# Optimization experiments

Hardware: AMD Instinct MI355X
Metric: run time of the kernel (lower is better)

The kernel has to match this reference:

```python
import jax, jax.numpy as jnp
import numpy as np
from jax import lax

BN_EPS = 1e-5


def _conv(x, w, b):
    # 3x3 conv, stride 1, padding 1 (SAME), NCHW/OIHW
    y = lax.conv_general_dilated(x, w, (1, 1), 'SAME',
                                 dimension_numbers=('NCHW', 'OIHW', 'NCHW'))
    return y + b[None, :, None, None]


def _bn(x, g, b, m, v):
    # eval-mode batchnorm with running stats
    scale = (g / jnp.sqrt(v + BN_EPS))[None, :, None, None]
    return (x - m[None, :, None, None]) * scale + b[None, :, None, None]


def _pool(x):
    # MaxPool2d(2,2), VALID (floor division of spatial dims)
    return lax.reduce_window(x, -jnp.inf, lax.max, (1, 1, 2, 2), (1, 1, 2, 2), 'VALID')


def _quantum(xq, qp):
    """Batched 5-qubit statevector sim of the PennyLane circuit.
    Wire i: RX(xq[:, i%2]) then RY(qp[i%2]); CNOT(0,1); CNOT(1,2); <Z0 Z1>.
    xq: [B, 32] (only first 2 features used). Returns [B] float32.
    """
    B = xq.shape[0]
    psi = jnp.zeros((B, 32), jnp.complex64).at[:, 0].set(1.0)
    for i in range(5):  # fixed tiny loop over wires
        a = xq[:, i % 2]          # [B] data angle
        th = qp[i % 2]            # scalar weight angle
        ca, sa = jnp.cos(a * 0.5), jnp.sin(a * 0.5)
        RX = jnp.stack([jnp.stack([ca, -1j * sa], -1),
                        jnp.stack([-1j * sa, ca], -1)], -2).astype(jnp.complex64)  # [B,2,2]
        cb, sb = jnp.cos(th * 0.5), jnp.sin(th * 0.5)
        RY = jnp.stack([jnp.stack([cb, -sb]), jnp.stack([sb, cb])]).astype(jnp.complex64)  # [2,2]
        U = jnp.einsum('ij,bjk->bik', RY, RX)  # [B,2,2] per-wire unitary
        psi = psi.reshape(B, 2 ** i, 2, 2 ** (4 - i))
        psi = jnp.einsum('bij,bajc->baic', U, psi).reshape(B, 32)
    psi = psi.reshape(B, 2, 2, 2, 2, 2)
    # CNOT(0,1): flip qubit 1 where qubit 0 == 1
    psi = psi.at[:, 1].set(psi[:, 1, ::-1])
    # CNOT(1,2): flip qubit 2 where qubit 1 == 1
    psi = psi.at[:, :, 1].set(psi[:, :, 1, ::-1])
    z01 = jnp.array([[1.0, -1.0], [-1.0, 1.0]], jnp.float32).reshape(1, 2, 2, 1, 1, 1)
    prob = jnp.real(psi) ** 2 + jnp.imag(psi) ** 2
    return jnp.sum(prob * z01, axis=(1, 2, 3, 4, 5))


def setup_inputs() -> dict:
    key = jax.random.key(0)
    ks = jax.random.split(key, 24)
    B = 8192
    s = 0.05
    d = {}
    d['x'] = jax.random.normal(ks[0], (B, 1, 28, 28), jnp.float32)
    d['conv1_w'] = jax.random.normal(ks[1], (64, 1, 3, 3), jnp.float32) * s
    d['conv1_b'] = jax.random.normal(ks[2], (64,), jnp.float32) * s
    d['conv2_w'] = jax.random.normal(ks[3], (128, 64, 3, 3), jnp.float32) * s
    d['conv2_b'] = jax.random.normal(ks[4], (128,), jnp.float32) * s
    d['conv3_w'] = jax.random.normal(ks[5], (256, 128, 3, 3), jnp.float32) * s
    d['conv3_b'] = jax.random.normal(ks[6], (256,), jnp.float32) * s
    for i, c in [(1, 64), (2, 128), (3, 256)]:
        d[f'bn{i}_g'] = jnp.ones((c,), jnp.float32)
        d[f'bn{i}_b'] = jnp.zeros((c,), jnp.float32)
        d[f'bn{i}_m'] = jax.random.normal(ks[6 + i], (c,), jnp.float32) * 0.1
        d[f'bn{i}_v'] = jax.random.uniform(ks[9 + i], (c,), jnp.float32, 0.5, 1.5)
    d['fc1_w'] = jax.random.normal(ks[13], (32, 256 * 3 * 3), jnp.float32) * s
    d['fc1_b'] = jax.random.normal(ks[14], (32,), jnp.float32) * s
    d['q_params'] = jax.random.uniform(ks[15], (8,), jnp.float32)
    d['fc2_w'] = jax.random.normal(ks[16], (128, 1), jnp.float32) * s
    d['fc2_b'] = jax.random.normal(ks[17], (128,), jnp.float32) * s
    d['fc3_w'] = jax.random.normal(ks[18], (2, 128), jnp.float32) * s
    d['fc3_b'] = jax.random.normal(ks[19], (2,), jnp.float32) * s
    return d


def reference(x, conv1_w, conv1_b, conv2_w, conv2_b, conv3_w, conv3_b,
              bn1_g, bn1_b, bn1_m, bn1_v, bn2_g, bn2_b, bn2_m, bn2_v,
              bn3_g, bn3_b, bn3_m, bn3_v, fc1_w, fc1_b, q_params,
              fc2_w, fc2_b, fc3_w, fc3_b):
    h = _pool(jax.nn.relu(_bn(_conv(x, conv1_w, conv1_b), bn1_g, bn1_b, bn1_m, bn1_v)))
    h = _pool(jax.nn.relu(_bn(_conv(h, conv2_w, conv2_b), bn2_g, bn2_b, bn2_m, bn2_v)))
    h = _pool(jax.nn.relu(_bn(_conv(h, conv3_w, conv3_b), bn3_g, bn3_b, bn3_m, bn3_v)))
    # dropout is identity in eval mode
    h = h.reshape(h.shape[0], -1)              # [B, 2304]
    h = h @ fc1_w.T + fc1_b                     # [B, 32]
    q = _quantum(h, q_params)[:, None]          # [B, 1]
    h = q @ fc2_w.T + fc2_b                     # [B, 128]
    logits = h @ fc3_w.T + fc3_b                # [B, 2]
    return jax.nn.log_softmax(logits, axis=1)
```

## Files before the change

kernel.cpp:

```cpp
#include <hip/hip_runtime.h>
#include <hip/hip_bf16.h>
#include <math.h>

typedef float f32x4 __attribute__((ext_vector_type(4)));
typedef short s16x8 __attribute__((ext_vector_type(8)));

static const long long OFF_W2  = 0LL;
static const long long OFF_W3  = 147456LL;
static const long long OFF_AB1 = 737280LL;
static const long long OFF_AB2 = 737792LL;
static const long long OFF_AB3 = 738816LL;
static const long long OFF_Q   = 740864LL;

__device__ inline unsigned short f2bfu(float f) {
    __hip_bfloat16 h = __float2bfloat16(f);
    unsigned short u;
    __builtin_memcpy(&u, &h, 2);
    return u;
}

__global__ __launch_bounds__(256) void prep_k(
    const float* __restrict__ c2w, const float* __restrict__ c3w,
    const float* __restrict__ c1b, const float* __restrict__ g1, const float* __restrict__ b1,
    const float* __restrict__ m1, const float* __restrict__ v1,
    const float* __restrict__ c2b, const float* __restrict__ g2, const float* __restrict__ b2,
    const float* __restrict__ m2, const float* __restrict__ v2,
    const float* __restrict__ c3b, const float* __restrict__ g3, const float* __restrict__ b3,
    const float* __restrict__ m3, const float* __restrict__ v3,
    const float* __restrict__ fc1b, const float* __restrict__ qp,
    const float* __restrict__ fc2w, const float* __restrict__ fc2b,
    const float* __restrict__ fc3w, const float* __restrict__ fc3b,
    short* __restrict__ wT2, short* __restrict__ wT3,
    float2* __restrict__ ab1, float2* __restrict__ ab2, float2* __restrict__ ab3,
    float* __restrict__ qc)
{
    int tid = blockIdx.x * 256 + threadIdx.x;
    if (tid < 73728) {
        int ic = tid & 63, oc = (tid >> 6) & 127, k = tid >> 13;
        wT2[tid] = (short)f2bfu(c2w[(oc * 64 + ic) * 9 + k]);
    }
    if (tid < 294912) {
        int ic = tid & 127, oc = (tid >> 7) & 255, k = tid >> 15;
        wT3[tid] = (short)f2bfu(c3w[(oc * 128 + ic) * 9 + k]);
    }
    if (tid < 64) {
        float s = g1[tid] / sqrtf(v1[tid] + 1e-5f);
        ab1[tid] = make_float2(s, (c1b[tid] - m1[tid]) * s + b1[tid]);
    } else if (tid < 192) {
        int c = tid - 64;
        float s = g2[c] / sqrtf(v2[c] + 1e-5f);
        ab2[c] = make_float2(s, (c2b[c] - m2[c]) * s + b2[c]);
    } else if (tid < 448) {
        int c = tid - 192;
        float s = g3[c] / sqrtf(v3[c] + 1e-5f);
        ab3[c] = make_float2(s, (c3b[c] - m3[c]) * s + b3[c]);
    } else if (tid == 448) {
        float A0 = 0.f, A1 = 0.f, B0 = 0.f, B1 = 0.f;
        for (int k = 0; k < 128; ++k) {
            float f2 = fc2w[k], fb = fc2b[k];
            A0 += fc3w[k] * f2;        B0 += fc3w[k] * fb;
            A1 += fc3w[128 + k] * f2;  B1 += fc3w[128 + k] * fb;
        }
        qc[0] = A0; qc[1] = A1;
        qc[2] = B0 + fc3b[0]; qc[3] = B1 + fc3b[1];
        qc[4] = cosf(qp[1]);  qc[5] = fc1b[1];
    }
}

__global__ __launch_bounds__(512, 6) void fused_k(
    const float* __restrict__ x, const float* __restrict__ c1w,
    const float2* __restrict__ ab1, const float2* __restrict__ ab2,
    const float2* __restrict__ ab3,
    const short* __restrict__ wT2, const short* __restrict__ wT3,
    const float* __restrict__ fc1w, const float* __restrict__ qc,
    float* __restrict__ out)
{
    __shared__ short xs2[16 * 16 * 64];
    __shared__ short u3[8 * 8 * 128];

    float (*xt)[32] = (float (*)[32])u3;
    short* xs3 = u3;
    float* red = (float*)u3;

    int b = blockIdx.x, t = threadIdx.x;

    for (int i = t; i < 8192; i += 512) ((unsigned*)xs2)[i] = 0u;
    for (int i = t; i < 960;  i += 512) ((unsigned*)u3)[i] = 0u;
    __syncthreads();

    for (int i = t; i < 784; i += 512) xt[i / 28 + 1][i % 28 + 1] = x[b * 784 + i];

    int ocg = t & 15;
    float wr[4][9];
    float2 abr[4];
#pragma unroll
    for (int c = 0; c < 4; ++c) {
#pragma unroll
        for (int k = 0; k < 9; ++k) wr[c][k] = c1w[(ocg * 4 + c) * 9 + k];
        abr[c] = ab1[ocg * 4 + c];
    }
    __syncthreads();

    int posb = t >> 4;
    for (int p = posb; p < 196; p += 32) {
        int py = p / 14, px = p % 14;
        int y0 = 2 * py, x0 = 2 * px;
        float patch[4][4];
#pragma unroll
        for (int i = 0; i < 4; ++i)
#pragma unroll
            for (int j = 0; j < 4; ++j) patch[i][j] = xt[y0 + i][x0 + j];

        unsigned short ub[4];
#pragma unroll
        for (int c = 0; c < 4; ++c) {
            float a00 = 0.f, a01 = 0.f, a10 = 0.f, a11 = 0.f;
#pragma unroll
            for (int ky = 0; ky < 3; ++ky)
#pragma unroll
                for (int kx = 0; kx < 3; ++kx) {
                    float wv = wr[c][ky * 3 + kx];
                    a00 += patch[ky + 0][kx + 0] * wv;
                    a01 += patch[ky + 0][kx + 1] * wv;
                    a10 += patch[ky + 1][kx + 0] * wv;
                    a11 += patch[ky + 1][kx + 1] * wv;
                }
            float aa = abr[c].x, bb = abr[c].y;
            float v = fmaxf(fmaxf(a00 * aa + bb, a01 * aa + bb),
                            fmaxf(a10 * aa + bb, a11 * aa + bb));
            ub[c] = f2bfu(fmaxf(v, 0.f));
        }
        uint2 pk;
        pk.x = (unsigned)ub[0] | ((unsigned)ub[1] << 16);
        pk.y = (unsigned)ub[2] | ((unsigned)ub[3] << 16);
        int blk = (ocg >> 1) ^ ((px + 1) & 7);
        *(uint2*)&xs2[((((py + 1) * 16) + (px + 1)) * 8 + blk) * 8 + (ocg & 1) * 4] = pk;
    }
    __syncthreads();
    for (int i = t; i < 960; i += 512) {
        int pos = i >> 6, w = i & 63;
        int yy = (pos < 8) ? 0 : pos - 7;
        int xx = (pos < 8) ? pos : 0;
        ((unsigned*)xs3)[(yy * 8 + xx) * 64 + w] = 0u;
    }

    int lane = t & 63, wid = t >> 6;
    int quad = lane >> 4, n16 = lane & 15;
    int dy = n16 >> 3, lx = n16 & 7;

    {
        f32x4 acc[14];
        f32x4 z = {0.f, 0.f, 0.f, 0.f};
#pragma unroll
        for (int nt = 0; nt < 14; ++nt) acc[nt] = z;

#pragma unroll 1
        for (int kykx = 0; kykx < 9; ++kykx) {
            int ky = kykx / 3, kx = kykx - 3 * ky;
            int dyky = dy + ky;
            int xc0 = lx + kx;
            int xc1 = xc0 + 8; if (xc1 > 15) xc1 = 15;
#pragma unroll
            for (int kk = 0; kk < 2; ++kk) {
                s16x8 A = *(const s16x8*)(wT2 + ((kykx * 128 + wid * 16 + n16) * 64 + kk * 32 + quad * 8));
                int bi = kk * 4 + quad;
#pragma unroll
                for (int nt = 0; nt < 14; ++nt) {
                    int ry = nt >> 1, cb = nt & 1;
                    int y_in = 2 * ry + dyky;
                    int x_in = cb ? xc1 : xc0;
                    int blk = bi ^ (x_in & 7);
                    s16x8 B = *(const s16x8*)&xs2[((y_in * 16 + x_in) * 8 + blk) * 8];
                    acc[nt] = __builtin_amdgcn_mfma_f32_16x16x32_bf16(A, B, acc[nt], 0, 0, 0);
                }
            }
        }

        int m = lx >> 1;
        bool keep = (dy == 0) && ((lx & 1) == 0);
        int oc0 = wid * 16 + quad * 4;
        float2 abv[4];
#pragma unroll
        for (int r = 0; r < 4; ++r) abv[r] = ab2[oc0 + r];
#pragma unroll
        for (int nt = 0; nt < 14; ++nt) {
            int ry = nt >> 1, cb = nt & 1;
            int xp = cb * 4 + m;
            float pv[4];
#pragma unroll
            for (int r = 0; r < 4; ++r) {
                float v = acc[nt][r] * abv[r].x + abv[r].y;
                v = fmaxf(v, __shfl_xor(v, 1));
                v = fmaxf(v, __shfl_xor(v, 8));
                pv[r] = fmaxf(v, 0.f);
            }
            if (keep && xp < 7) {
                uint2 pk;
                pk.x = (unsigned)f2bfu(pv[0]) | ((unsigned)f2bfu(pv[1]) << 16);
                pk.y = (unsigned)f2bfu(pv[2]) | ((unsigned)f2bfu(pv[3]) << 16);
                int blk3 = (oc0 >> 3) ^ (((xp + 1) & 7) << 1);
                *(uint2*)&xs3[(((ry + 1) * 8 + (xp + 1)) * 16 + blk3) * 8 + (oc0 & 7)] = pk;
            }
        }
    }
    __syncthreads();

    f32x4 acc[2][3];
    f32x4 z = {0.f, 0.f, 0.f, 0.f};
#pragma unroll
    for (int ml = 0; ml < 2; ++ml)
#pragma unroll
        for (int nt = 0; nt < 3; ++nt) acc[ml][nt] = z;

#pragma unroll 1
    for (int kykx = 0; kykx < 9; ++kykx) {
        int ky = kykx / 3, kx = kykx - 3 * ky;
        int dyky = dy + ky;
        int x_in = lx + kx; if (x_in > 7) x_in = 7;
#pragma unroll
        for (int kk = 0; kk < 4; ++kk) {
            s16x8 A[2];
#pragma unroll
            for (int ml = 0; ml < 2; ++ml)
                A[ml] = *(const s16x8*)(wT3 + ((kykx * 256 + (wid * 2 + ml) * 16 + n16) * 128 + kk * 32 + quad * 8));
            int bi = kk * 4 + quad;
            int blk = bi ^ ((x_in & 7) << 1);
#pragma unroll
            for (int nt = 0; nt < 3; ++nt) {
                int y_in = 2 * nt + dyky;
                s16x8 B = *(const s16x8*)&xs3[((y_in * 8 + x_in) * 16 + blk) * 8];
#pragma unroll
                for (int ml = 0; ml < 2; ++ml)
                    acc[ml][nt] = __builtin_amdgcn_mfma_f32_16x16x32_bf16(A[ml], B, acc[ml][nt], 0, 0, 0);
            }
        }
    }
    __syncthreads();

    float vacc = 0.f;
    int m = lx >> 1;
    bool keep = (dy == 0) && ((lx & 1) == 0) && (m < 3);
    const float* fc1w1 = fc1w + 2304;
#pragma unroll
    for (int ml = 0; ml < 2; ++ml) {
        int oc0 = (wid * 2 + ml) * 16 + quad * 4;
        float2 abv[4];
#pragma unroll
        for (int r = 0; r < 4; ++r) abv[r] = ab3[oc0 + r];
#pragma unroll
        for (int nt = 0; nt < 3; ++nt) {
#pragma unroll
            for (int r = 0; r < 4; ++r) {
                float v = acc[ml][nt][r] * abv[r].x + abv[r].y;
                v = fmaxf(v, __shfl_xor(v, 1));
                v = fmaxf(v, __shfl_xor(v, 8));
                v = fmaxf(v, 0.f);
                if (keep) vacc += v * fc1w1[(oc0 + r) * 9 + nt * 3 + m];
            }
        }
    }
#pragma unroll
    for (int s = 1; s < 64; s <<= 1) vacc += __shfl_xor(vacc, s);
    if (lane == 0) red[wid] = vacc;
    __syncthreads();
    if (t == 0) {
        float v = red[0] + red[1] + red[2] + red[3]
                + red[4] + red[5] + red[6] + red[7] + qc[5];
        float q = cosf(v) * qc[4];
        float l0 = q * qc[0] + qc[2];
        float l1 = q * qc[1] + qc[3];
        float mx = fmaxf(l0, l1);
        float lse = mx + logf(__expf(l0 - mx) + __expf(l1 - mx));
        out[b * 2 + 0] = l0 - lse;
        out[b * 2 + 1] = l1 - lse;
    }
}

extern "C" void kernel_launch(void* const* d_in, const int* in_sizes, int n_in,
                              void* d_out, int out_size, void* d_ws, size_t ws_size,
                              hipStream_t stream)
{
    const float* x    = (const float*)d_in[0];
    const float* c1w  = (const float*)d_in[1];
    const float* c1b  = (const float*)d_in[2];
    const float* c2w  = (const float*)d_in[3];
    const float* c2b  = (const float*)d_in[4];
    const float* c3w  = (const float*)d_in[5];
    const float* c3b  = (const float*)d_in[6];
    const float* g1   = (const float*)d_in[7];
    const float* b1   = (const float*)d_in[8];
    const float* m1   = (const float*)d_in[9];
    const float* v1   = (const float*)d_in[10];
    const float* g2   = (const float*)d_in[11];
    const float* b2   = (const float*)d_in[12];
    const float* m2   = (const float*)d_in[13];
    const float* v2   = (const float*)d_in[14];
    const float* g3   = (const float*)d_in[15];
    const float* b3   = (const float*)d_in[16];
    const float* m3   = (const float*)d_in[17];
    const float* v3   = (const float*)d_in[18];
    const float* fc1w = (const float*)d_in[19];
    const float* fc1b = (const float*)d_in[20];
    const float* qp   = (const float*)d_in[21];
    const float* fc2w = (const float*)d_in[22];
    const float* fc2b = (const float*)d_in[23];
    const float* fc3w = (const float*)d_in[24];
    const float* fc3b = (const float*)d_in[25];
    float* out = (float*)d_out;
    char* ws = (char*)d_ws;

    short*  wT2 = (short*)(ws + OFF_W2);
    short*  wT3 = (short*)(ws + OFF_W3);
    float2* ab1 = (float2*)(ws + OFF_AB1);
    float2* ab2 = (float2*)(ws + OFF_AB2);
    float2* ab3 = (float2*)(ws + OFF_AB3);
    float*  qc  = (float*)(ws + OFF_Q);

    int B = in_sizes[0] / 784;

    prep_k<<<1152, 256, 0, stream>>>(c2w, c3w, c1b, g1, b1, m1, v1,
                                     c2b, g2, b2, m2, v2, c3b, g3, b3, m3, v3,
                                     fc1b, qp, fc2w, fc2b, fc3w, fc3b,
                                     wT2, wT3, ab1, ab2, ab3, qc);
    fused_k<<<B, 512, 0, stream>>>(x, c1w, ab1, ab2, ab3, wT2, wT3, fc1w, qc, out);
}
```

Baseline: 935.2 us.

## Compute conv1 with bf16 MFMA and fold BN into weights

Replaces the scalar FP32 conv1+BN+ReLU+pool loop with a bf16 MFMA 16x16x32 formulation. The BN scale is folded into the weights and the shift enters as a bias row against a constant-one input. The 2x2 max-pool is done with lane shuffles across the MFMA output columns. The input loads are also hoisted before the shared-memory zeroing to overlap latency. This adds bf16 rounding of the input pixels and of the BN-scaled weights, which were previously FP32, so it risks a small accuracy loss.

Measured after the change: 1.289 ms. 1.38x slower.

```diff
diff --git a/kernel.cpp b/kernel.cpp
--- a/kernel.cpp
+++ b/kernel.cpp
@@ -83,58 +83,82 @@
     float* red = (float*)u3;
 
     int b = blockIdx.x, t = threadIdx.x;
+    int lane = t & 63, wid = t >> 6;
+    int n16 = lane & 15, quad = lane >> 4;
+    int dy = n16 >> 3, lx = n16 & 7;
+
+    float xv0 = x[b * 784 + t];
+    float xv1 = (t + 512 < 784) ? x[b * 784 + t + 512] : 0.f;
+
+    s16x8 A1f[4];
+#pragma unroll
+    for (int ot = 0; ot < 4; ++ot) {
+        float2 ab = ab1[ot * 16 + n16];
+        s16x8 a = {0, 0, 0, 0, 0, 0, 0, 0};
+        if (quad == 0) {
+#pragma unroll
+            for (int j = 0; j < 8; ++j)
+                a[j] = (short)f2bfu(c1w[(ot * 16 + n16) * 9 + j] * ab.x);
+        } else if (quad == 1) {
+            a[0] = (short)f2bfu(c1w[(ot * 16 + n16) * 9 + 8] * ab.x);
+            a[1] = (short)f2bfu(ab.y);
+        }
+        A1f[ot] = a;
+    }
 
     for (int i = t; i < 8192; i += 512) ((unsigned*)xs2)[i] = 0u;
     for (int i = t; i < 960;  i += 512) ((unsigned*)u3)[i] = 0u;
     __syncthreads();
 
-    for (int i = t; i < 784; i += 512) xt[i / 28 + 1][i % 28 + 1] = x[b * 784 + i];
-
-    int ocg = t & 15;
-    float wr[4][9];
-    float2 abr[4];
-#pragma unroll
-    for (int c = 0; c < 4; ++c) {
-#pragma unroll
-        for (int k = 0; k < 9; ++k) wr[c][k] = c1w[(ocg * 4 + c) * 9 + k];
-        abr[c] = ab1[ocg * 4 + c];
-    }
-    __syncthreads();
-
-    int posb = t >> 4;
-    for (int p = posb; p < 196; p += 32) {
-        int py = p / 14, px = p % 14;
-        int y0 = 2 * py, x0 = 2 * px;
-        float patch[4][4];
-#pragma unroll
-        for (int i = 0; i < 4; ++i)
-#pragma unroll
-            for (int j = 0; j < 4; ++j) patch[i][j] = xt[y0 + i][x0 + j];
-
-        unsigned short ub[4];
-#pragma unroll
-        for (int c = 0; c < 4; ++c) {
-            float a00 = 0.f, a01 = 0.f, a10 = 0.f, a11 = 0.f;
-#pragma unroll
-            for (int ky = 0; ky < 3; ++ky)
-#pragma unroll
-                for (int kx = 0; kx < 3; ++kx) {
-                    float wv = wr[c][ky * 3 + kx];
-                    a00 += patch[ky + 0][kx + 0] * wv;
-                    a01 += patch[ky + 0][kx + 1] * wv;
-                    a10 += patch[ky + 1][kx + 0] * wv;
-                    a11 += patch[ky + 1][kx + 1] * wv;
-                }
-            float aa = abr[c].x, bb = abr[c].y;
-            float v = fmaxf(fmaxf(a00 * aa + bb, a01 * aa + bb),
-                            fmaxf(a10 * aa + bb, a11 * aa + bb));
-            ub[c] = f2bfu(fmaxf(v, 0.f));
-        }
-        uint2 pk;
-        pk.x = (unsigned)ub[0] | ((unsigned)ub[1] << 16);
-        pk.y = (unsigned)ub[2] | ((unsigned)ub[3] << 16);
-        int blk = (ocg >> 1) ^ ((px + 1) & 7);
-        *(uint2*)&xs2[((((py + 1) * 16) + (px + 1)) * 8 + blk) * 8 + (ocg & 1) * 4] = pk;
+    xt[t / 28 + 1][t % 28 + 1] = xv0;
+    if (t + 512 < 784) xt[(t + 512) / 28 + 1][(t + 512) % 28 + 1] = xv1;
+    __syncthreads();
+
+    for (int T = wid; T < 49; T += 8) {
+        int q = T * 4 + (n16 >> 2);
+        int qy = q / 14, qx = q - qy * 14;
+        int yy = 2 * qy + ((n16 >> 1) & 1);
+        int xx = 2 * qx + (n16 & 1);
+        const float* pxt = &xt[yy][xx];
+        s16x8 Bf = {0, 0, 0, 0, 0, 0, 0, 0};
+        if (quad == 0) {
+            Bf[0] = (short)f2bfu(pxt[0]);
+            Bf[1] = (short)f2bfu(pxt[1]);
+            Bf[2] = (short)f2bfu(pxt[2]);
+            Bf[3] = (short)f2bfu(pxt[32]);
+            Bf[4] = (short)f2bfu(pxt[33]);
+            Bf[5] = (short)f2bfu(pxt[34]);
+            Bf[6] = (short)f2bfu(pxt[64]);
+            Bf[7] = (short)f2bfu(pxt[65]);
+        } else if (quad == 1) {
+            Bf[0] = (short)f2bfu(pxt[66]);
+            Bf[1] = (short)0x3F80;
+        }
+
+        f32x4 z4 = {0.f, 0.f, 0.f, 0.f};
+        bool wr = ((n16 & 3) == 0);
+        int wb = (qy + 1) * 16 + (qx + 1);
+        int blkb = (qx + 1) & 7;
+#pragma unroll
+        for (int ot = 0; ot < 4; ++ot) {
+            f32x4 acc = __builtin_amdgcn_mfma_f32_16x16x32_bf16(A1f[ot], Bf, z4, 0, 0, 0);
+            unsigned short us[4];
+#pragma unroll
+            for (int r = 0; r < 4; ++r) {
+                float v = acc[r];
+                v = fmaxf(v, __shfl_xor(v, 1));
+                v = fmaxf(v, __shfl_xor(v, 2));
+                us[r] = f2bfu(fmaxf(v, 0.f));
+            }
+            if (wr) {
+                int oc0 = ot * 16 + quad * 4;
+                uint2 pk;
+                pk.x = (unsigned)us[0] | ((unsigned)us[1] << 16);
+                pk.y = (unsigned)us[2] | ((unsigned)us[3] << 16);
+                int blk = (oc0 >> 3) ^ blkb;
+                *(uint2*)&xs2[((wb * 8) + blk) * 8 + (oc0 & 7)] = pk;
+            }
+        }
     }
     __syncthreads();
     for (int i = t; i < 960; i += 512) {
@@ -143,10 +167,6 @@
         int xx = (pos < 8) ? pos : 0;
         ((unsigned*)xs3)[(yy * 8 + xx) * 64 + w] = 0u;
     }
-
-    int lane = t & 63, wid = t >> 6;
-    int quad = lane >> 4, n16 = lane & 15;
-    int dy = n16 >> 3, lx = n16 & 7;
 
     {
         f32x4 acc[14];
```
